# Kernel tuning notes

Hardware: AMD Instinct MI355X
Metric: run time of the kernel (lower is better)

The kernel has to match this reference:

```python
import jax, jax.numpy as jnp
import numpy as np

DIM = 2048
N_HEADS = 32
N_KV_HEADS = 8
HEAD_DIM = DIM // N_HEADS  # 64
N_REP = N_HEADS // N_KV_HEADS  # 4
SEQ = 2048
BSZ = 1


def _rope(x, cos, sin):
    # x: [b, s, h, hd]; cos/sin: [s, hd//2]
    x2 = x.reshape(*x.shape[:-1], HEAD_DIM // 2, 2)
    xe, xo = x2[..., 0], x2[..., 1]
    c = cos[None, :, None, :]
    s = sin[None, :, None, :]
    oe = xe * c - xo * s
    oo = xe * s + xo * c
    return jnp.stack([oe, oo], axis=-1).reshape(x.shape)


def setup_inputs() -> dict:
    key = jax.random.key(0)
    ks = jax.random.split(key, 6)
    x = jax.random.normal(ks[0], (BSZ, SEQ, DIM), dtype=jnp.float32)
    # llama-style rotary freqs
    inv = 1.0 / (10000.0 ** (np.arange(0, HEAD_DIM, 2, dtype=np.float32) / HEAD_DIM))
    t = np.arange(SEQ, dtype=np.float32)
    ang = np.outer(t, inv)  # [s, hd//2]
    freqs_cos = jnp.asarray(np.cos(ang))
    freqs_sin = jnp.asarray(np.sin(ang))
    # additive causal mask
    mask = jnp.where(jnp.tril(jnp.ones((SEQ, SEQ), bool)), 0.0, -jnp.inf).astype(jnp.float32)
    sc = 1.0 / np.sqrt(DIM)
    wq = jax.random.normal(ks[1], (DIM, N_HEADS * HEAD_DIM), jnp.float32) * sc
    wk = jax.random.normal(ks[2], (DIM, N_KV_HEADS * HEAD_DIM), jnp.float32) * sc
    wv = jax.random.normal(ks[3], (DIM, N_KV_HEADS * HEAD_DIM), jnp.float32) * sc
    wo = jax.random.normal(ks[4], (N_HEADS * HEAD_DIM, DIM), jnp.float32) * sc
    return {"x": x, "freqs_cos": freqs_cos, "freqs_sin": freqs_sin, "mask": mask,
            "wq": wq, "wk": wk, "wv": wv, "wo": wo}


def reference(x, freqs_cos, freqs_sin, mask, wq, wk, wv, wo):
    b, s, _ = x.shape
    xq = (x @ wq).reshape(b, s, N_HEADS, HEAD_DIM)
    xk = (x @ wk).reshape(b, s, N_KV_HEADS, HEAD_DIM)
    xv = (x @ wv).reshape(b, s, N_KV_HEADS, HEAD_DIM)
    xq = _rope(xq, freqs_cos, freqs_sin)
    xk = _rope(xk, freqs_cos, freqs_sin)
    # repeat_kv: expand kv heads by n_rep
    xk = jnp.repeat(xk, N_REP, axis=2)  # [b, s, H, hd]
    xv = jnp.repeat(xv, N_REP, axis=2)
    scores = jnp.einsum('bqhd,bkhd->bhqk', xq, xk) / np.sqrt(HEAD_DIM)
    scores = scores + mask[None, None, :, :]
    probs = jax.nn.softmax(scores.astype(jnp.float32), axis=-1).astype(xq.dtype)
    out = jnp.einsum('bhqk,bkhd->bqhd', probs, xv).reshape(b, s, N_HEADS * HEAD_DIM)
    return out @ wo
```

## Files before the change

kernel.cpp:

```cpp
#include <hip/hip_runtime.h>
#include <hip/hip_bf16.h>

#define SEQ  2048
#define DIM  2048
#define NQK  3072
#define NH   32
#define NKV  8
#define HD   64
#define SCL  0.18033688f

typedef __attribute__((ext_vector_type(8))) short s8v;
typedef __attribute__((ext_vector_type(4))) short s4v;
typedef __attribute__((ext_vector_type(4))) float f32x4;

__device__ __forceinline__ short f2bf_bits(float f) {
    __hip_bfloat16 b = __float2bfloat16(f);
    short s; __builtin_memcpy(&s, &b, 2); return s;
}
__device__ __forceinline__ float bfbits2f(short s) {
    __hip_bfloat16 b; __builtin_memcpy(&b, &s, 2);
    return __bfloat162float(b);
}
__device__ __forceinline__ f32x4 mfma16(s8v a, s8v b, f32x4 c) {
    return __builtin_amdgcn_mfma_f32_16x16x32_bf16(a, b, c, 0, 0, 0);
}
__device__ __forceinline__ void load16_to_lds(const void* g, void* l) {
    __builtin_amdgcn_global_load_lds(
        (const __attribute__((address_space(1))) void*)g,
        (__attribute__((address_space(3))) void*)l, 16, 0, 0);
}
__device__ __forceinline__ float fexp2(float x) {
    float y; asm("v_exp_f32 %0, %1" : "=v"(y) : "v"(x)); return y;
}

__global__ void cvt_f32_bf16(const float* __restrict__ src, short* __restrict__ dst) {
    int i = (blockIdx.x * 256 + threadIdx.x) * 4;
    float4 v = *(const float4*)(src + i);
    s4v o;
    o.x = f2bf_bits(v.x); o.y = f2bf_bits(v.y);
    o.z = f2bf_bits(v.z); o.w = f2bf_bits(v.w);
    *(s4v*)(dst + i) = o;
}

__global__ void transpose_cvt(const float* __restrict__ src, short* __restrict__ dst, int Cs) {
    __shared__ float tile[32][33];
    int bx = blockIdx.x * 32, by = blockIdx.y * 32;
    int tx = threadIdx.x, ty = threadIdx.y;
    #pragma unroll
    for (int j = 0; j < 32; j += 8)
        tile[ty + j][tx] = src[(size_t)(by + ty + j) * Cs + bx + tx];
    __syncthreads();
    #pragma unroll
    for (int j = 0; j < 32; j += 8)
        dst[(size_t)(bx + ty + j) * 2048 + by + tx] = f2bf_bits(tile[tx][ty + j]);
}

template<int S>
__global__ __launch_bounds__(256, 3)
void gemm_bt(const short* __restrict__ A, const short* __restrict__ BT,
             short* __restrict__ P0, short* __restrict__ P1, short* __restrict__ P2,
             int N, int K, int nx)
{
    __shared__ short As[128 * 64];
    __shared__ short Bs[128 * 64];
    const int nwg = gridDim.x;
    const int orig = blockIdx.x;
    const int wg = (orig & 7) * (nwg >> 3) + (orig >> 3);
    const int per = nwg / S;
    const int ks  = wg / per;
    const int bxy = wg - ks * per;
    const int bm = (bxy / nx) * 128, bn = (bxy % nx) * 128;
    const int kslice = ((K / S) + 63) & ~63;
    const int kbeg = ks * kslice;
    const int kend = (kbeg + kslice < K) ? (kbeg + kslice) : K;

    const int lane = threadIdx.x & 63;
    const int wid  = threadIdx.x >> 6;
    const int r = lane & 15, g = lane >> 4;
    const int wm = (wid >> 1) * 64, wn = (wid & 1) * 64;

    f32x4 acc[4][4];
    #pragma unroll
    for (int i = 0; i < 4; ++i)
        #pragma unroll
        for (int j = 0; j < 4; ++j) acc[i][j] = (f32x4){0.f, 0.f, 0.f, 0.f};

    const int srow = wid * 32 + (lane >> 3);
    const int scol = (lane & 7) * 8;

    for (int k0 = kbeg; k0 < kend; k0 += 64) {
        #pragma unroll
        for (int s2 = 0; s2 < 4; ++s2) {
            int row = srow + s2 * 8;
            int seg = wid * 4 + s2;
            load16_to_lds(A  + (size_t)(bm + row) * K + k0 + scol, As + seg * 512);
            load16_to_lds(BT + (size_t)(bn + row) * K + k0 + scol, Bs + seg * 512);
        }
        __syncthreads();
        #pragma unroll
        for (int kk = 0; kk < 64; kk += 32) {
            s8v a[4], b[4];
            #pragma unroll
            for (int t = 0; t < 4; ++t)
                a[t] = *(const s8v*)&As[(wm + t * 16 + r) * 64 + kk + g * 8];
            #pragma unroll
            for (int t = 0; t < 4; ++t)
                b[t] = *(const s8v*)&Bs[(wn + t * 16 + r) * 64 + kk + g * 8];
            __builtin_amdgcn_s_setprio(1);
            #pragma unroll
            for (int i = 0; i < 4; ++i)
                #pragma unroll
                for (int j = 0; j < 4; ++j)
                    acc[i][j] = mfma16(a[i], b[j], acc[i][j]);
            __builtin_amdgcn_s_setprio(0);
        }
        __syncthreads();
    }

    short* P = (ks == 0) ? P0 : ((ks == 1) ? P1 : P2);
    #pragma unroll
    for (int i = 0; i < 4; ++i)
        #pragma unroll
        for (int j = 0; j < 4; ++j)
            #pragma unroll
            for (int q = 0; q < 4; ++q) {
                int row = bm + wm + i * 16 + g * 4 + q;
                int col = bn + wn + j * 16 + r;
                P[(size_t)row * N + col] = f2bf_bits(acc[i][j][q]);
            }
}

__global__ void rope_add(const short* __restrict__ P0, const short* __restrict__ P1,
                         short* __restrict__ qkv,
                         const float* __restrict__ fc, const float* __restrict__ fs) {
    int idx = blockIdx.x * 256 + threadIdx.x;
    int row = idx / 320;
    int col = (idx - row * 320) * 8;
    s8v a = *(const s8v*)(P0 + (size_t)row * NQK + col);
    s8v b = *(const s8v*)(P1 + (size_t)row * NQK + col);
    int p0 = (col & 63) >> 1;
    float scl = (col < 2048) ? SCL : 1.0f;
    s8v o;
    #pragma unroll
    for (int k = 0; k < 4; ++k) {
        float xe = bfbits2f(a[2 * k])     + bfbits2f(b[2 * k]);
        float xo = bfbits2f(a[2 * k + 1]) + bfbits2f(b[2 * k + 1]);
        float c  = fc[row * 32 + p0 + k];
        float sn = fs[row * 32 + p0 + k];
        o[2 * k]     = f2bf_bits((xe * c - xo * sn) * scl);
        o[2 * k + 1] = f2bf_bits((xe * sn + xo * c) * scl);
    }
    *(s8v*)(qkv + (size_t)row * NQK + col) = o;
}

__global__ void vT_add(const short* __restrict__ P0, const short* __restrict__ P1,
                       short* __restrict__ vT) {
    __shared__ float tile[32][33];
    int bx = blockIdx.x * 32;
    int by = blockIdx.y * 32;
    int tx = threadIdx.x, ty = threadIdx.y;
    #pragma unroll
    for (int j = 0; j < 32; j += 8) {
        size_t off = (size_t)(by + ty + j) * NQK + 2560 + bx + tx;
        tile[ty + j][tx] = bfbits2f(P0[off]) + bfbits2f(P1[off]);
    }
    __syncthreads();
    #pragma unroll
    for (int j = 0; j < 32; j += 8)
        vT[(size_t)(bx + ty + j) * 2048 + by + tx] = f2bf_bits(tile[tx][ty + j]);
}

__global__ void add_out3(const short* __restrict__ R0, const short* __restrict__ R1,
                         const short* __restrict__ R2, float* __restrict__ out) {
    int i = (blockIdx.x * 256 + threadIdx.x) * 8;
    s8v a = *(const s8v*)(R0 + i);
    s8v b = *(const s8v*)(R1 + i);
    s8v c = *(const s8v*)(R2 + i);
    #pragma unroll
    for (int k = 0; k < 8; k += 4) {
        float4 o;
        o.x = bfbits2f(a[k])     + bfbits2f(b[k])     + bfbits2f(c[k]);
        o.y = bfbits2f(a[k + 1]) + bfbits2f(b[k + 1]) + bfbits2f(c[k + 1]);
        o.z = bfbits2f(a[k + 2]) + bfbits2f(b[k + 2]) + bfbits2f(c[k + 2]);
        o.w = bfbits2f(a[k + 3]) + bfbits2f(b[k + 3]) + bfbits2f(c[k + 3]);
        *(float4*)(out + i + k) = o;
    }
}

__global__ __launch_bounds__(256, 5)
void flash_attn(const short* __restrict__ qkv, const short* __restrict__ vT,
                short* __restrict__ O) {
    const int h  = blockIdx.x;
    const int qi = (int)gridDim.y - 1 - (int)blockIdx.y;
    const int qb = qi * 64;
    const int kh = h >> 2;
    const int lane = threadIdx.x & 63;
    const int wid  = threadIdx.x >> 6;
    const int r = lane & 15, g = lane >> 4;

    __shared__ short Ks[64][72];
    __shared__ short Vt[64][72];
    __shared__ short Pl[4][16][72];

    s8v qf0, qf1;
    {
        const short* qrow = qkv + (size_t)(qb + wid * 16 + r) * NQK + h * 64;
        qf0 = *(const s8v*)(qrow + g * 8);
        qf1 = *(const s8v*)(qrow + 32 + g * 8);
    }

    float mrow = -1e30f, lrow = 0.f;
    f32x4 o[4];
    #pragma unroll
    for (int t = 0; t < 4; ++t) o[t] = (f32x4){0.f, 0.f, 0.f, 0.f};

    const int tr = threadIdx.x >> 2;
    const int tc = (threadIdx.x & 3) * 16;

    {
        const short* kg = qkv + (size_t)(tr) * NQK + 2048 + kh * 64 + tc;
        *(s8v*)&Ks[tr][tc]     = *(const s8v*)kg;
        *(s8v*)&Ks[tr][tc + 8] = *(const s8v*)(kg + 8);
        const short* vg = vT + (size_t)(kh * 64 + tr) * 2048 + tc;
        *(s8v*)&Vt[tr][tc]     = *(const s8v*)vg;
        *(s8v*)&Vt[tr][tc + 8] = *(const s8v*)(vg + 8);
    }
    __syncthreads();

    const int nkt = qi + 1;
    for (int kt = 0; kt < nkt; ++kt) {
        const bool more = (kt + 1 < nkt);
        s8v kn0, kn1, vn0, vn1;
        if (more) {
            const short* kg = qkv + (size_t)((kt + 1) * 64 + tr) * NQK + 2048 + kh * 64 + tc;
            kn0 = *(const s8v*)kg;
            kn1 = *(const s8v*)(kg + 8);
            const short* vg = vT + (size_t)(kh * 64 + tr) * 2048 + (kt + 1) * 64 + tc;
            vn0 = *(const s8v*)vg;
            vn1 = *(const s8v*)(vg + 8);
        }

        f32x4 s[4];
        __builtin_amdgcn_s_setprio(1);
        #pragma unroll
        for (int t = 0; t < 4; ++t) {
            s8v ka0 = *(const s8v*)&Ks[t * 16 + r][g * 8];
            s8v ka1 = *(const s8v*)&Ks[t * 16 + r][32 + g * 8];
            f32x4 z = (f32x4){0.f, 0.f, 0.f, 0.f};
            z = mfma16(ka0, qf0, z);
            z = mfma16(ka1, qf1, z);
            s[t] = z;
        }
        __builtin_amdgcn_s_setprio(0);

        if (kt == nkt - 1) {
            const int qrow = qb + wid * 16 + r;
            #pragma unroll
            for (int t = 0; t < 4; ++t)
                #pragma unroll
                for (int q = 0; q < 4; ++q)
                    if (kt * 64 + t * 16 + g * 4 + q > qrow) s[t][q] = -1e30f;
        }

        float pm = fmaxf(fmaxf(fmaxf(s[0][0], s[0][1]), fmaxf(s[0][2], s[0][3])),
                         fmaxf(fmaxf(s[1][0], s[1][1]), fmaxf(s[1][2], s[1][3])));
        pm = fmaxf(pm, fmaxf(fmaxf(fmaxf(s[2][0], s[2][1]), fmaxf(s[2][2], s[2][3])),
                             fmaxf(fmaxf(s[3][0], s[3][1]), fmaxf(s[3][2], s[3][3]))));
        pm = fmaxf(pm, __shfl_xor(pm, 16, 64));
        pm = fmaxf(pm, __shfl_xor(pm, 32, 64));

        if (__any(pm > mrow + 8.f)) {
            float mn = fmaxf(mrow, pm);
            float al = fexp2(mrow - mn);
            mrow = mn;
            lrow *= al;
            float alq[4];
            #pragma unroll
            for (int q = 0; q < 4; ++q) alq[q] = __shfl(al, g * 4 + q, 64);
            #pragma unroll
            for (int t = 0; t < 4; ++t)
                #pragma unroll
                for (int q = 0; q < 4; ++q) o[t][q] *= alq[q];
        }

        float rs = 0.f;
        #pragma unroll
        for (int t = 0; t < 4; ++t)
            #pragma unroll
            for (int q = 0; q < 4; ++q) {
                float p = fexp2(s[t][q] - mrow);
                s[t][q] = p;
                rs += p;
            }
        rs += __shfl_xor(rs, 16, 64);
        rs += __shfl_xor(rs, 32, 64);
        lrow += rs;

        #pragma unroll
        for (int t = 0; t < 4; ++t) {
            s4v pk;
            #pragma unroll
            for (int q = 0; q < 4; ++q) pk[q] = f2bf_bits(s[t][q]);
            *(s4v*)&Pl[wid][r][t * 16 + g * 4] = pk;
        }
        asm volatile("s_waitcnt lgkmcnt(0)" ::: "memory");

        s8v pa0 = *(const s8v*)&Pl[wid][r][g * 8];
        s8v pa1 = *(const s8v*)&Pl[wid][r][32 + g * 8];
        __builtin_amdgcn_s_setprio(1);
        #pragma unroll
        for (int t = 0; t < 4; ++t) {
            s8v vb0 = *(const s8v*)&Vt[t * 16 + r][g * 8];
            s8v vb1 = *(const s8v*)&Vt[t * 16 + r][32 + g * 8];
            o[t] = mfma16(pa0, vb0, o[t]);
            o[t] = mfma16(pa1, vb1, o[t]);
        }
        __builtin_amdgcn_s_setprio(0);
        __syncthreads();

        if (more) {
            *(s8v*)&Ks[tr][tc]     = kn0;
            *(s8v*)&Ks[tr][tc + 8] = kn1;
            *(s8v*)&Vt[tr][tc]     = vn0;
            *(s8v*)&Vt[tr][tc + 8] = vn1;
            __syncthreads();
        }
    }

    float rl = __builtin_amdgcn_rcpf(lrow);
    float rlq[4];
    #pragma unroll
    for (int q = 0; q < 4; ++q) rlq[q] = __shfl(rl, g * 4 + q, 64);
    #pragma unroll
    for (int t = 0; t < 4; ++t)
        #pragma unroll
        for (int q = 0; q < 4; ++q)
            O[(size_t)(qb + wid * 16 + g * 4 + q) * 2048 + h * 64 + t * 16 + r] =
                f2bf_bits(o[t][q] * rlq[q]);
}

extern "C" void kernel_launch(void* const* d_in, const int* in_sizes, int n_in,
                              void* d_out, int out_size, void* d_ws, size_t ws_size,
                              hipStream_t stream)
{
    const float* x  = (const float*)d_in[0];
    const float* fc = (const float*)d_in[1];
    const float* fs = (const float*)d_in[2];
    const float* wq = (const float*)d_in[4];
    const float* wk = (const float*)d_in[5];
    const float* wv = (const float*)d_in[6];
    const float* wo = (const float*)d_in[7];
    float* out = (float*)d_out;

    char* ws = (char*)d_ws;
    short* xb    = (short*)(ws);
    short* wqkvT = (short*)(ws + 8  * 1024 * 1024);
    short* woT   = (short*)(ws + 20 * 1024 * 1024);
    short* qkv   = (short*)(ws + 28 * 1024 * 1024);
    short* vT    = (short*)(ws + 40 * 1024 * 1024);
    short* attnO = (short*)(ws + 42 * 1024 * 1024);
    short* P0    = (short*)(ws + 50 * 1024 * 1024);
    short* P1    = (short*)(ws + 63 * 1024 * 1024);
    short* P2o   = qkv;

    dim3 tb(32, 8);
    cvt_f32_bf16<<<4096, 256, 0, stream>>>(x, xb);
    transpose_cvt<<<dim3(64, 64), tb, 0, stream>>>(wq, wqkvT, 2048);
    transpose_cvt<<<dim3(16, 64), tb, 0, stream>>>(wk, wqkvT + 2048 * 2048, 512);
    transpose_cvt<<<dim3(16, 64), tb, 0, stream>>>(wv, wqkvT + 2560 * 2048, 512);
    transpose_cvt<<<dim3(64, 64), tb, 0, stream>>>(wo, woT, 2048);

    gemm_bt<2><<<768, 256, 0, stream>>>(xb, wqkvT, P0, P1, nullptr, 3072, 2048, 24);
    rope_add<<<2560, 256, 0, stream>>>(P0, P1, qkv, fc, fs);
    vT_add<<<dim3(16, 64), tb, 0, stream>>>(P0, P1, vT);

    flash_attn<<<dim3(32, 32), 256, 0, stream>>>(qkv, vT, attnO);

    gemm_bt<3><<<768, 256, 0, stream>>>(attnO, woT, P0, P1, P2o, 2048, 2048, 16);
    add_out3<<<2048, 256, 0, stream>>>(P0, P1, P2o, out);
}
```

Before: 246.6 us.

## Merge prep and epilogue kernels, double-buffer attention K/V, split output GEMM four ways

Folds the five conversion and transpose launches into one prep kernel and the rope and V-transpose epilogues into one kernel, cutting launch count and tail gaps. The flash attention loop now double-buffers K/V in LDS and writes the next tile before the PV stage, which removes one barrier per iteration. Occupancy hint drops from 5 to 3 blocks per CU to make room for the extra LDS. The output projection uses split-K of 4 (1024 workgroups) with a four-way add, trading extra partial-sum traffic for better CU fill.

```diff
diff --git a/kernel.cpp b/kernel.cpp
--- a/kernel.cpp
+++ b/kernel.cpp
@@ -33,19 +33,30 @@
     float y; asm("v_exp_f32 %0, %1" : "=v"(y) : "v"(x)); return y;
 }
 
-__global__ void cvt_f32_bf16(const float* __restrict__ src, short* __restrict__ dst) {
-    int i = (blockIdx.x * 256 + threadIdx.x) * 4;
-    float4 v = *(const float4*)(src + i);
-    s4v o;
-    o.x = f2bf_bits(v.x); o.y = f2bf_bits(v.y);
-    o.z = f2bf_bits(v.z); o.w = f2bf_bits(v.w);
-    *(s4v*)(dst + i) = o;
-}
-
-__global__ void transpose_cvt(const float* __restrict__ src, short* __restrict__ dst, int Cs) {
+__global__ void prep(const float* __restrict__ x,
+                     const float* __restrict__ wq, const float* __restrict__ wk,
+                     const float* __restrict__ wv, const float* __restrict__ wo,
+                     short* __restrict__ xb, short* __restrict__ wqkvT, short* __restrict__ woT)
+{
     __shared__ float tile[32][33];
-    int bx = blockIdx.x * 32, by = blockIdx.y * 32;
-    int tx = threadIdx.x, ty = threadIdx.y;
+    int b = blockIdx.x;
+    int tid = threadIdx.x;
+    if (b < 4096) {
+        int i = (b * 256 + tid) * 4;
+        float4 v = *(const float4*)(x + i);
+        s4v o;
+        o.x = f2bf_bits(v.x); o.y = f2bf_bits(v.y);
+        o.z = f2bf_bits(v.z); o.w = f2bf_bits(v.w);
+        *(s4v*)(xb + i) = o;
+        return;
+    }
+    b -= 4096;
+    const float* src; short* dst; int Cs, bx, by;
+    if (b < 4096)      {             src = wq; dst = wqkvT;              Cs = 2048; bx = (b & 63) * 32; by = (b >> 6) * 32; }
+    else if (b < 5120) { int j = b - 4096; src = wk; dst = wqkvT + 2048 * 2048; Cs = 512; bx = (j & 15) * 32; by = (j >> 4) * 32; }
+    else if (b < 6144) { int j = b - 5120; src = wv; dst = wqkvT + 2560 * 2048; Cs = 512; bx = (j & 15) * 32; by = (j >> 4) * 32; }
+    else               { int j = b - 6144; src = wo; dst = woT;               Cs = 2048; bx = (j & 63) * 32; by = (j >> 6) * 32; }
+    int tx = tid & 31, ty = tid >> 5;
     #pragma unroll
     for (int j = 0; j < 32; j += 8)
         tile[ty + j][tx] = src[(size_t)(by + ty + j) * Cs + bx + tx];
@@ -58,7 +69,8 @@
 template<int S>
 __global__ __launch_bounds__(256, 3)
 void gemm_bt(const short* __restrict__ A, const short* __restrict__ BT,
-             short* __restrict__ P0, short* __restrict__ P1, short* __restrict__ P2,
+             short* __restrict__ P0, short* __restrict__ P1,
+             short* __restrict__ P2, short* __restrict__ P3,
              int N, int K, int nx)
 {
     __shared__ short As[128 * 64];
@@ -70,9 +82,8 @@
     const int ks  = wg / per;
     const int bxy = wg - ks * per;
     const int bm = (bxy / nx) * 128, bn = (bxy % nx) * 128;
-    const int kslice = ((K / S) + 63) & ~63;
-    const int kbeg = ks * kslice;
-    const int kend = (kbeg + kslice < K) ? (kbeg + kslice) : K;
+    const int kslice = K / S;
+    const int kbeg = ks * kslice, kend = kbeg + kslice;
 
     const int lane = threadIdx.x & 63;
     const int wid  = threadIdx.x >> 6;
@@ -117,7 +128,10 @@
         __syncthreads();
     }
 
-    short* P = (ks == 0) ? P0 : ((ks == 1) ? P1 : P2);
+    short* P = P0;
+    if (S >= 2 && ks == 1) P = P1;
+    if (S >= 3 && ks == 2) P = P2;
+    if (S >= 4 && ks == 3) P = P3;
     #pragma unroll
     for (int i = 0; i < 4; ++i)
         #pragma unroll
@@ -130,64 +144,70 @@
             }
 }
 
-__global__ void rope_add(const short* __restrict__ P0, const short* __restrict__ P1,
-                         short* __restrict__ qkv,
-                         const float* __restrict__ fc, const float* __restrict__ fs) {
-    int idx = blockIdx.x * 256 + threadIdx.x;
-    int row = idx / 320;
-    int col = (idx - row * 320) * 8;
-    s8v a = *(const s8v*)(P0 + (size_t)row * NQK + col);
-    s8v b = *(const s8v*)(P1 + (size_t)row * NQK + col);
-    int p0 = (col & 63) >> 1;
-    float scl = (col < 2048) ? SCL : 1.0f;
-    s8v o;
-    #pragma unroll
-    for (int k = 0; k < 4; ++k) {
-        float xe = bfbits2f(a[2 * k])     + bfbits2f(b[2 * k]);
-        float xo = bfbits2f(a[2 * k + 1]) + bfbits2f(b[2 * k + 1]);
-        float c  = fc[row * 32 + p0 + k];
-        float sn = fs[row * 32 + p0 + k];
-        o[2 * k]     = f2bf_bits((xe * c - xo * sn) * scl);
-        o[2 * k + 1] = f2bf_bits((xe * sn + xo * c) * scl);
-    }
-    *(s8v*)(qkv + (size_t)row * NQK + col) = o;
-}
-
-__global__ void vT_add(const short* __restrict__ P0, const short* __restrict__ P1,
-                       short* __restrict__ vT) {
+__global__ void ep1(const short* __restrict__ P0, const short* __restrict__ P1,
+                    short* __restrict__ qkv, short* __restrict__ vT,
+                    const float* __restrict__ fc, const float* __restrict__ fs)
+{
     __shared__ float tile[32][33];
-    int bx = blockIdx.x * 32;
-    int by = blockIdx.y * 32;
-    int tx = threadIdx.x, ty = threadIdx.y;
-    #pragma unroll
-    for (int j = 0; j < 32; j += 8) {
-        size_t off = (size_t)(by + ty + j) * NQK + 2560 + bx + tx;
-        tile[ty + j][tx] = bfbits2f(P0[off]) + bfbits2f(P1[off]);
-    }
-    __syncthreads();
-    #pragma unroll
-    for (int j = 0; j < 32; j += 8)
-        vT[(size_t)(bx + ty + j) * 2048 + by + tx] = f2bf_bits(tile[tx][ty + j]);
-}
-
-__global__ void add_out3(const short* __restrict__ R0, const short* __restrict__ R1,
-                         const short* __restrict__ R2, float* __restrict__ out) {
+    int b = blockIdx.x;
+    int tid = threadIdx.x;
+    if (b < 2560) {
+        int idx = b * 256 + tid;
+        int row = idx / 320;
+        int col = (idx - row * 320) * 8;
+        s8v a = *(const s8v*)(P0 + (size_t)row * NQK + col);
+        s8v bb = *(const s8v*)(P1 + (size_t)row * NQK + col);
+        int p0 = (col & 63) >> 1;
+        float scl = (col < 2048) ? SCL : 1.0f;
+        s8v o;
+        #pragma unroll
+        for (int k = 0; k < 4; ++k) {
+            float xe = bfbits2f(a[2 * k])     + bfbits2f(bb[2 * k]);
+            float xo = bfbits2f(a[2 * k + 1]) + bfbits2f(bb[2 * k + 1]);
+            float c  = fc[row * 32 + p0 + k];
+            float sn = fs[row * 32 + p0 + k];
+            o[2 * k]     = f2bf_bits((xe * c - xo * sn) * scl);
+            o[2 * k + 1] = f2bf_bits((xe * sn + xo * c) * scl);
+        }
+        *(s8v*)(qkv + (size_t)row * NQK + col) = o;
+        return;
+    }
+    {
+        int j = b - 2560;
+        int bx = (j & 15) * 32, by = (j >> 4) * 32;
+        int tx = tid & 31, ty = tid >> 5;
+        #pragma unroll
+        for (int jj = 0; jj < 32; jj += 8) {
+            size_t off = (size_t)(by + ty + jj) * NQK + 2560 + bx + tx;
+            tile[ty + jj][tx] = bfbits2f(P0[off]) + bfbits2f(P1[off]);
+        }
+        __syncthreads();
+        #pragma unroll
+        for (int jj = 0; jj < 32; jj += 8)
+            vT[(size_t)(bx + ty + jj) * 2048 + by + tx] = f2bf_bits(tile[tx][ty + jj]);
+    }
+}
+
+__global__ void add_out4(const short* __restrict__ R0, const short* __restrict__ R1,
+                         const short* __restrict__ R2, const short* __restrict__ R3,
+                         float* __restrict__ out) {
     int i = (blockIdx.x * 256 + threadIdx.x) * 8;
     s8v a = *(const s8v*)(R0 + i);
     s8v b = *(const s8v*)(R1 + i);
     s8v c = *(const s8v*)(R2 + i);
+    s8v d = *(const s8v*)(R3 + i);
     #pragma unroll
     for (int k = 0; k < 8; k += 4) {
         float4 o;
-        o.x = bfbits2f(a[k])     + bfbits2f(b[k])     + bfbits2f(c[k]);
-        o.y = bfbits2f(a[k + 1]) + bfbits2f(b[k + 1]) + bfbits2f(c[k + 1]);
-        o.z = bfbits2f(a[k + 2]) + bfbits2f(b[k + 2]) + bfbits2f(c[k + 2]);
-        o.w = bfbits2f(a[k + 3]) + bfbits2f(b[k + 3]) + bfbits2f(c[k + 3]);
+        o.x = (bfbits2f(a[k])     + bfbits2f(b[k]))     + (bfbits2f(c[k])     + bfbits2f(d[k]));
+        o.y = (bfbits2f(a[k + 1]) + bfbits2f(b[k + 1])) + (bfbits2f(c[k + 1]) + bfbits2f(d[k + 1]));
+        o.z = (bfbits2f(a[k + 2]) + bfbits2f(b[k + 2])) + (bfbits2f(c[k + 2]) + bfbits2f(d[k + 2]));
+        o.w = (bfbits2f(a[k + 3]) + bfbits2f(b[k + 3])) + (bfbits2f(c[k + 3]) + bfbits2f(d[k + 3]));
         *(float4*)(out + i + k) = o;
     }
 }
 
-__global__ __launch_bounds__(256, 5)
+__global__ __launch_bounds__(256, 3)
 void flash_attn(const short* __restrict__ qkv, const short* __restrict__ vT,
                 short* __restrict__ O) {
     const int h  = blockIdx.x;
@@ -198,8 +218,8 @@
     const int wid  = threadIdx.x >> 6;
     const int r = lane & 15, g = lane >> 4;
 
-    __shared__ short Ks[64][72];
-    __shared__ short Vt[64][72];
+    __shared__ short Ks[2][64][72];
+    __shared__ short Vt[2][64][72];
     __shared__ short Pl[4][16][72];
 
     s8v qf0, qf1;
@@ -218,17 +238,18 @@
     const int tc = (threadIdx.x & 3) * 16;
 
     {
-        const short* kg = qkv + (size_t)(tr) * NQK + 2048 + kh * 64 + tc;
-        *(s8v*)&Ks[tr][tc]     = *(const s8v*)kg;
-        *(s8v*)&Ks[tr][tc + 8] = *(const s8v*)(kg + 8);
+        const short* kg = qkv + (size_t)tr * NQK + 2048 + kh * 64 + tc;
+        *(s8v*)&Ks[0][tr][tc]     = *(const s8v*)kg;
+        *(s8v*)&Ks[0][tr][tc + 8] = *(const s8v*)(kg + 8);
         const short* vg = vT + (size_t)(kh * 64 + tr) * 2048 + tc;
-        *(s8v*)&Vt[tr][tc]     = *(const s8v*)vg;
-        *(s8v*)&Vt[tr][tc + 8] = *(const s8v*)(vg + 8);
+        *(s8v*)&Vt[0][tr][tc]     = *(const s8v*)vg;
+        *(s8v*)&Vt[0][tr][tc + 8] = *(const s8v*)(vg + 8);
     }
     __syncthreads();
 
     const int nkt = qi + 1;
     for (int kt = 0; kt < nkt; ++kt) {
+        const int cur = kt & 1;
         const bool more = (kt + 1 < nkt);
         s8v kn0, kn1, vn0, vn1;
         if (more) {
@@ -244,8 +265,8 @@
         __builtin_amdgcn_s_setprio(1);
         #pragma unroll
         for (int t = 0; t < 4; ++t) {
-            s8v ka0 = *(const s8v*)&Ks[t * 16 + r][g * 8];
-            s8v ka1 = *(const s8v*)&Ks[t * 16 + r][32 + g * 8];
+            s8v ka0 = *(const s8v*)&Ks[cur][t * 16 + r][g * 8];
+            s8v ka1 = *(const s8v*)&Ks[cur][t * 16 + r][32 + g * 8];
             f32x4 z = (f32x4){0.f, 0.f, 0.f, 0.f};
             z = mfma16(ka0, qf0, z);
             z = mfma16(ka1, qf1, z);
@@ -303,6 +324,13 @@
             for (int q = 0; q < 4; ++q) pk[q] = f2bf_bits(s[t][q]);
             *(s4v*)&Pl[wid][r][t * 16 + g * 4] = pk;
         }
+
+        if (more) {
+            *(s8v*)&Ks[cur ^ 1][tr][tc]     = kn0;
+            *(s8v*)&Ks[cur ^ 1][tr][tc + 8] = kn1;
+            *(s8v*)&Vt[cur ^ 1][tr][tc]     = vn0;
+            *(s8v*)&Vt[cur ^ 1][tr][tc + 8] = vn1;
+        }
         asm volatile("s_waitcnt lgkmcnt(0)" ::: "memory");
 
         s8v pa0 = *(const s8v*)&Pl[wid][r][g * 8];
@@ -310,21 +338,13 @@
         __builtin_amdgcn_s_setprio(1);
         #pragma unroll
         for (int t = 0; t < 4; ++t) {
-            s8v vb0 = *(const s8v*)&Vt[t * 16 + r][g * 8];
-            s8v vb1 = *(const s8v*)&Vt[t * 16 + r][32 + g * 8];
+            s8v vb0 = *(const s8v*)&Vt[cur][t * 16 + r][g * 8];
+            s8v vb1 = *(const s8v*)&Vt[cur][t * 16 + r][32 + g * 8];
             o[t] = mfma16(pa0, vb0, o[t]);
             o[t] = mfma16(pa1, vb1, o[t]);
         }
         __builtin_amdgcn_s_setprio(0);
         __syncthreads();
-
-        if (more) {
-            *(s8v*)&Ks[tr][tc]     = kn0;
-            *(s8v*)&Ks[tr][tc + 8] = kn1;
-            *(s8v*)&Vt[tr][tc]     = vn0;
-            *(s8v*)&Vt[tr][tc + 8] = vn1;
-            __syncthreads();
-        }
     }
 
     float rl = __builtin_amdgcn_rcpf(lrow);
@@ -361,21 +381,14 @@
     short* attnO = (short*)(ws + 42 * 1024 * 1024);
     short* P0    = (short*)(ws + 50 * 1024 * 1024);
     short* P1    = (short*)(ws + 63 * 1024 * 1024);
-    short* P2o   = qkv;
-
-    dim3 tb(32, 8);
-    cvt_f32_bf16<<<4096, 256, 0, stream>>>(x, xb);
-    transpose_cvt<<<dim3(64, 64), tb, 0, stream>>>(wq, wqkvT, 2048);
-    transpose_cvt<<<dim3(16, 64), tb, 0, stream>>>(wk, wqkvT + 2048 * 2048, 512);
-    transpose_cvt<<<dim3(16, 64), tb, 0, stream>>>(wv, wqkvT + 2560 * 2048, 512);
-    transpose_cvt<<<dim3(64, 64), tb, 0, stream>>>(wo, woT, 2048);
-
-    gemm_bt<2><<<768, 256, 0, stream>>>(xb, wqkvT, P0, P1, nullptr, 3072, 2048, 24);
-    rope_add<<<2560, 256, 0, stream>>>(P0, P1, qkv, fc, fs);
-    vT_add<<<dim3(16, 64), tb, 0, stream>>>(P0, P1, vT);
+
+    prep<<<14336, 256, 0, stream>>>(x, wq, wk, wv, wo, xb, wqkvT, woT);
+
+    gemm_bt<2><<<768, 256, 0, stream>>>(xb, wqkvT, P0, P1, nullptr, nullptr, 3072, 2048, 24);
+    ep1<<<3584, 256, 0, stream>>>(P0, P1, qkv, vT, fc, fs);
 
     flash_attn<<<dim3(32, 32), 256, 0, stream>>>(qkv, vT, attnO);
 
-    gemm_bt<3><<<768, 256, 0, stream>>>(attnO, woT, P0, P1, P2o, 2048, 2048, 16);
-    add_out3<<<2048, 256, 0, stream>>>(P0, P1, P2o, out);
-}
+    gemm_bt<4><<<1024, 256, 0, stream>>>(attnO, woT, P0, P1, qkv, xb, 2048, 2048, 16);
+    add_out4<<<2048, 256, 0, stream>>>(P0, P1, qkv, xb, out);
+}
```

Result: faster. 235.8 us (-4.4%).
